# Optimization experiments

Hardware: AMD Instinct MI355X
Metric: run time of the kernel (lower is better)

## Reference

```python
import jax, jax.numpy as jnp
import numpy as np

N = 50000          # num nodes
E = 800000         # num edges
NEG_SLOPE = 0.2    # leaky relu slope for attention logits


def gat_layer(h, W, al, ar, src, dst, res_W=None, res_identity=False, apply_elu=False):
    """One GATConv layer (DGL semantics, dropout=0, fc bias-free).
    h: [N, F_in]; W: [F_in, H*D]; al, ar: [H, D]. Returns [N, H, D]."""
    H, D = al.shape
    feat = (h @ W).reshape(N, H, D)                      # projected features
    el = jnp.sum(feat * al, axis=-1)                     # [N, H]
    er = jnp.sum(feat * ar, axis=-1)                     # [N, H]
    e = jax.nn.leaky_relu(el[src] + er[dst], NEG_SLOPE)  # [E, H] edge logits
    # numerically-stable edge softmax segmented over destination nodes
    m = jax.ops.segment_max(e, dst, num_segments=N)      # [N, H]
    m = jnp.where(jnp.isfinite(m), m, 0.0)               # nodes with no in-edges
    ex = jnp.exp(e - m[dst])
    den = jax.ops.segment_sum(ex, dst, num_segments=N)   # [N, H]
    alpha = ex / (den[dst] + 1e-9)                       # [E, H]
    # message passing: gather src feats, weight by alpha, scatter-add to dst
    out = jax.ops.segment_sum(feat[src] * alpha[..., None], dst, num_segments=N)
    if res_identity:
        out = out + h.reshape(N, H, D)
    elif res_W is not None:
        out = out + (h @ res_W).reshape(N, H, D)
    if apply_elu:
        out = jax.nn.elu(out)
    return out


def setup_inputs() -> dict:
    key = jax.random.key(0)
    ks = jax.random.split(key, 14)
    s = 0.1  # keep attention logits tame
    return {
        "features": jax.random.normal(ks[0], (N, 128), jnp.float32),
        "W0": jax.random.normal(ks[1], (128, 128), jnp.float32) * s,
        "al0": jax.random.normal(ks[2], (4, 32), jnp.float32) * s,
        "ar0": jax.random.normal(ks[3], (4, 32), jnp.float32) * s,
        "W1": jax.random.normal(ks[4], (128, 128), jnp.float32) * s,
        "al1": jax.random.normal(ks[5], (4, 32), jnp.float32) * s,
        "ar1": jax.random.normal(ks[6], (4, 32), jnp.float32) * s,
        "W2": jax.random.normal(ks[7], (128, 40), jnp.float32) * s,
        "al2": jax.random.normal(ks[8], (1, 40), jnp.float32) * s,
        "ar2": jax.random.normal(ks[9], (1, 40), jnp.float32) * s,
        "resW2": jax.random.normal(ks[10], (128, 40), jnp.float32) * s,
        "src": jax.random.randint(ks[11], (E,), 0, N, jnp.int32),
        "dst": jax.random.randint(ks[12], (E,), 0, N, jnp.int32),
    }


def reference(features, W0, al0, ar0, W1, al1, ar1, W2, al2, ar2, resW2, src, dst):
    # hidden layer 0: no residual, elu, flatten heads
    h = gat_layer(features, W0, al0, ar0, src, dst, apply_elu=True).reshape(N, -1)
    # hidden layer 1: residual (identity since in == heads*out), elu, flatten
    h = gat_layer(h, W1, al1, ar1, src, dst, res_identity=True, apply_elu=True).reshape(N, -1)
    # output layer: residual projection, no activation, mean over heads
    logits = gat_layer(h, W2, al2, ar2, src, dst, res_W=resW2).mean(axis=1)
    return logits
```

## Files before the change

### kernel.cpp

```cpp
#include <hip/hip_runtime.h>
#include <hip/hip_fp16.h>

#define NNODES 50000
#define NEDGES 800000
#define NBUCK 196
#define NCHUNK 256
#define CHUNK 3125

typedef _Float16 f16x8 __attribute__((ext_vector_type(8)));
typedef float f32x4 __attribute__((ext_vector_type(4)));


__global__ __launch_bounds__(256) void k_packhist(const int* __restrict__ src,
                                                  const int* __restrict__ dst,
                                                  unsigned* __restrict__ pack,
                                                  int* __restrict__ hist) {
  __shared__ int h[NBUCK];
  int t = threadIdx.x, c = blockIdx.x;
  for (int i = t; i < NBUCK; i += 256) h[i] = 0;
  __syncthreads();
  int beg = c * CHUNK;
  for (int q = t; q < CHUNK; q += 256) {
    int e = beg + q;
    unsigned d = (unsigned)dst[e], sv = (unsigned)src[e];
    pack[e] = (d << 16) | sv;
    atomicAdd(&h[d >> 8], 1);
  }
  __syncthreads();
  for (int i = t; i < NBUCK; i += 256) hist[i * NCHUNK + c] = h[i];
}

__global__ __launch_bounds__(1024) void k_scanall(const int* __restrict__ hist,
                                                  int* __restrict__ off) {
  __shared__ int sb[1024];
  int t = threadIdx.x;
  const int P = (NBUCK * NCHUNK) / 1024;
  int base = t * P;
  int s = 0;
  for (int i = 0; i < P; ++i) s += hist[base + i];
  sb[t] = s;
  __syncthreads();
  for (int o = 1; o < 1024; o <<= 1) {
    int x = (t >= o) ? sb[t - o] : 0;
    __syncthreads();
    sb[t] += x;
    __syncthreads();
  }
  int ex = sb[t] - s;
  for (int i = 0; i < P; ++i) {
    int v = hist[base + i];
    off[base + i] = ex;
    ex += v;
  }
}

__global__ __launch_bounds__(256) void k_partition(const unsigned* __restrict__ pack,
                                                   const int* __restrict__ off,
                                                   unsigned* __restrict__ bucketed) {
  __shared__ int cur[NBUCK];
  int t = threadIdx.x, c = blockIdx.x;
  for (int i = t; i < NBUCK; i += 256) cur[i] = off[i * NCHUNK + c];
  __syncthreads();
  int beg = c * CHUNK;
  for (int q = t; q < CHUNK; q += 256) {
    unsigned v = pack[beg + q];
    int pos = atomicAdd(&cur[v >> 24], 1);
    bucketed[pos] = v;
  }
}

__global__ __launch_bounds__(256) void k_sortbkt(const unsigned* __restrict__ bucketed,
                                                 const int* __restrict__ off,
                                                 int* __restrict__ row_off,
                                                 int* __restrict__ esrc) {
  __shared__ int cnt[256];
  __shared__ int cur[256];
  int t = threadIdx.x, b = blockIdx.x;
  int base = off[b * NCHUNK];
  int endb = (b == NBUCK - 1) ? NEDGES : off[(b + 1) * NCHUNK];
  int ne = endb - base;
  cnt[t] = 0;
  __syncthreads();
  for (int i = t; i < ne; i += 256)
    atomicAdd(&cnt[(bucketed[base + i] >> 16) & 255], 1);
  __syncthreads();
  int orig = cnt[t];
  cur[t] = orig;
  __syncthreads();
  for (int o = 1; o < 256; o <<= 1) {
    int x = (t >= o) ? cur[t - o] : 0;
    __syncthreads();
    cur[t] += x;
    __syncthreads();
  }
  int excl = cur[t] - orig;
  int g = (b << 8) + t;
  if (g <= NNODES) row_off[g] = base + excl;
  cur[t] = excl;
  __syncthreads();
  for (int i = t; i < ne; i += 256) {
    unsigned v = bucketed[base + i];
    int pos = base + atomicAdd(&cur[(v >> 16) & 255], 1);
    esrc[pos] = (int)(v & 0xFFFFu);
  }
}

__global__ __launch_bounds__(128) void k_prep(const float* __restrict__ W0, const float* __restrict__ al0,
                                              const float* __restrict__ ar0,
                                              const float* __restrict__ W1, const float* __restrict__ al1,
                                              const float* __restrict__ ar1,
                                              const float* __restrict__ W2, const float* __restrict__ resW2,
                                              const float* __restrict__ al2, const float* __restrict__ ar2,
                                              _Float16* __restrict__ Wt0, _Float16* __restrict__ Wt1,
                                              _Float16* __restrict__ Wt2) {
  int b = blockIdx.x, k = threadIdx.x;
  if (b < 288) {
    const float* W = (b < 144) ? W0 : W1;
    const float* al = (b < 144) ? al0 : al1;
    const float* ar = (b < 144) ? ar0 : ar1;
    _Float16* Wt = (b < 144) ? Wt0 : Wt1;
    int c = (b < 144) ? b : b - 144;
    float v = 0.f;
    if (c < 128) {
      v = W[k * 128 + c];
    } else if (c < 136) {
      int h = c - 128;
      const float* av = (h < 4) ? al : ar;
      int hh = h & 3;
      float s = 0.f;
      for (int d = 0; d < 32; ++d) s += W[k * 128 + hh * 32 + d] * av[hh * 32 + d];
      v = s;
    }
    Wt[c * 128 + k] = (_Float16)v;
  } else {
    int c = b - 288;
    float v = 0.f;
    if (c < 40) {
      v = W2[k * 40 + c];
    } else if (c < 80) {
      v = resW2[k * 40 + (c - 40)];
    } else if (c == 80) {
      float s = 0.f;
      for (int d = 0; d < 40; ++d) s += W2[k * 40 + d] * al2[d];
      v = s;
    } else if (c == 81) {
      float s = 0.f;
      for (int d = 0; d < 40; ++d) s += W2[k * 40 + d] * ar2[d];
      v = s;
    }
    Wt2[c * 128 + k] = (_Float16)v;
  }
}

template <int NCT, bool L2E, bool AF32>
__global__ __launch_bounds__(512) void k_gemm_mfma(const void* __restrict__ Av,
                                                   const _Float16* __restrict__ Wtg,
                                                   __half* __restrict__ C,
                                                   float* __restrict__ resOut,
                                                   float* __restrict__ el,
                                                   float* __restrict__ er, int nrows) {
  __shared__ _Float16 Ah[128 * 136];
  __shared__ _Float16 Wl[NCT * 16 * 136];
  int t = threadIdx.x;
  int r0 = blockIdx.x * 128;

  for (int q = t; q < NCT * 16 * 16; q += 512) {
    int row = q >> 4, k8 = (q & 15) * 8;
    *(f16x8*)(&Wl[row * 136 + k8]) = *(const f16x8*)(Wtg + row * 128 + k8);
  }
  if (AF32) {
    const float* A = (const float*)Av;
    #pragma unroll
    for (int p = 0; p < 8; ++p) {
      int q = p * 512 + t;
      int r = q >> 5, k4 = (q & 31) * 4;
      float4 v = make_float4(0.f, 0.f, 0.f, 0.f);
      if (r0 + r < nrows) v = *(const float4*)(A + (size_t)(r0 + r) * 128 + k4);
      union { _Float16 h[4]; uint2 u; } pk;
      pk.h[0] = (_Float16)v.x; pk.h[1] = (_Float16)v.y;
      pk.h[2] = (_Float16)v.z; pk.h[3] = (_Float16)v.w;
      *(uint2*)(&Ah[r * 136 + k4]) = pk.u;
    }
  } else {
    const __half* A = (const __half*)Av;
    #pragma unroll
    for (int p = 0; p < 4; ++p) {
      int q = p * 512 + t;
      int r = q >> 4, k8 = (q & 15) * 8;
      union { f16x8 v; uint4 u; } pk;
      pk.u = make_uint4(0, 0, 0, 0);
      if (r0 + r < nrows) pk.v = *(const f16x8*)(A + (size_t)(r0 + r) * 128 + k8);
      *(f16x8*)(&Ah[r * 136 + k8]) = pk.v;
    }
  }
  __syncthreads();

  int wave = t >> 6, l = t & 63;
  const _Float16* abase = &Ah[(wave * 16 + (l & 15)) * 136 + ((l >> 4) * 8)];
  const _Float16* bbase = &Wl[(l & 15) * 136 + ((l >> 4) * 8)];

  f32x4 acc[NCT] = {};
  #pragma unroll
  for (int ks = 0; ks < 4; ++ks) {
    f16x8 af = *(const f16x8*)(abase + ks * 32);
    #pragma unroll
    for (int nt = 0; nt < NCT; ++nt) {
      f16x8 bf = *(const f16x8*)(bbase + nt * 16 * 136 + ks * 32);
      acc[nt] = __builtin_amdgcn_mfma_f32_16x16x32_f16(af, bf, acc[nt], 0, 0, 0);
    }
  }

  int cc = l & 15;
  int rbase = r0 + wave * 16 + (l >> 4) * 4;
  #pragma unroll
  for (int r = 0; r < 4; ++r) {
    int row = rbase + r;
    if (row >= nrows) continue;
    if (!L2E) {
      #pragma unroll
      for (int nt = 0; nt < 8; ++nt)
        C[(size_t)row * 128 + nt * 16 + cc] = __float2half_rn(acc[nt][r]);
      float v = acc[8][r];
      if (cc < 4) el[row * 4 + cc] = v;
      else if (cc < 8) er[row * 4 + (cc - 4)] = v;
    } else {
      #pragma unroll
      for (int nt = 0; nt < 6; ++nt) {
        int col = nt * 16 + cc;
        float v = acc[nt][r];
        if (col < 40) C[(size_t)row * 40 + col] = __float2half_rn(v);
        else if (col < 80) resOut[(size_t)row * 40 + (col - 40)] = v;
        else if (col == 80) el[row] = v;
        else if (col == 81) er[row] = v;
      }
    }
  }
}

__device__ __forceinline__ void fma8h(float4& a0, float4& a1, float w, const uint4& r) {
  const __half* hp = (const __half*)&r;
  a0.x += w * __half2float(hp[0]);
  a0.y += w * __half2float(hp[1]);
  a0.z += w * __half2float(hp[2]);
  a0.w += w * __half2float(hp[3]);
  a1.x += w * __half2float(hp[4]);
  a1.y += w * __half2float(hp[5]);
  a1.z += w * __half2float(hp[6]);
  a1.w += w * __half2float(hp[7]);
}

template <bool RES, bool DOELU>
__global__ __launch_bounds__(256) void k_msg128v5(const __half* __restrict__ feat,
                                                  const float* __restrict__ el,
                                                  const float* __restrict__ er,
                                                  const int* __restrict__ row_off,
                                                  const int* __restrict__ esrc,
                                                  const __half* __restrict__ hres,
                                                  __half* __restrict__ out, int nnodes) {
  int t = threadIdx.x;
  int n = blockIdx.x * 16 + (t >> 4);
  if (n >= nnodes) return;
  int lane = t & 15;
  int h = lane >> 2;
  int s = row_off[n], e = row_off[n + 1];
  float ern = er[n * 4 + h];
  float4 acc0[4] = {}, acc1[4] = {};
  float dpart = 0.f;
  int hb = h << 2;

  for (int c = s; c < e; c += 16) {
    int m = e - c; if (m > 16) m = 16;
    int sjl = (lane < m) ? esrc[c + lane] : 0;
    int b0 = lane & 3;
    int e0 = __shfl(sjl, b0, 16);
    int e1 = __shfl(sjl, b0 + 4, 16);
    int e2 = __shfl(sjl, b0 + 8, 16);
    int e3 = __shfl(sjl, b0 + 12, 16);
    float x0 = el[e0 * 4 + h] + ern;
    float x1 = el[e1 * 4 + h] + ern;
    float x2 = el[e2 * 4 + h] + ern;
    float x3 = el[e3 * 4 + h] + ern;
    x0 = fmaxf(x0, 0.2f * x0);
    x1 = fmaxf(x1, 0.2f * x1);
    x2 = fmaxf(x2, 0.2f * x2);
    x3 = fmaxf(x3, 0.2f * x3);
    float w0 = (b0 < m) ? __expf(x0) : 0.f;
    float w1 = (b0 + 4 < m) ? __expf(x1) : 0.f;
    float w2 = (b0 + 8 < m) ? __expf(x2) : 0.f;
    float w3 = (b0 + 12 < m) ? __expf(x3) : 0.f;
    dpart += (w0 + w1) + (w2 + w3);

#define GAT_J(J, WK)                                                          \
    if (J < m) {                                                              \
      float wgt = __shfl(WK, hb | (J & 3), 16);                               \
      int sj = __shfl(sjl, J, 16);                                            \
      uint4 raw = *(const uint4*)(feat + (size_t)sj * 128 + lane * 8);        \
      fma8h(acc0[J & 3], acc1[J & 3], wgt, raw);                              \
    }
    GAT_J(0, w0) GAT_J(1, w0) GAT_J(2, w0) GAT_J(3, w0)
    GAT_J(4, w1) GAT_J(5, w1) GAT_J(6, w1) GAT_J(7, w1)
    GAT_J(8, w2) GAT_J(9, w2) GAT_J(10, w2) GAT_J(11, w2)
    GAT_J(12, w3) GAT_J(13, w3) GAT_J(14, w3) GAT_J(15, w3)
#undef GAT_J
  }

  float den = dpart;
  den += __shfl_xor(den, 1, 16);
  den += __shfl_xor(den, 2, 16);

  float4 A0, A1;
  A0.x = (acc0[0].x + acc0[1].x) + (acc0[2].x + acc0[3].x);
  A0.y = (acc0[0].y + acc0[1].y) + (acc0[2].y + acc0[3].y);
  A0.z = (acc0[0].z + acc0[1].z) + (acc0[2].z + acc0[3].z);
  A0.w = (acc0[0].w + acc0[1].w) + (acc0[2].w + acc0[3].w);
  A1.x = (acc1[0].x + acc1[1].x) + (acc1[2].x + acc1[3].x);
  A1.y = (acc1[0].y + acc1[1].y) + (acc1[2].y + acc1[3].y);
  A1.z = (acc1[0].z + acc1[1].z) + (acc1[2].z + acc1[3].z);
  A1.w = (acc1[0].w + acc1[1].w) + (acc1[2].w + acc1[3].w);
  float inv = (e > s) ? 1.f / den : 0.f;
  A0.x *= inv; A0.y *= inv; A0.z *= inv; A0.w *= inv;
  A1.x *= inv; A1.y *= inv; A1.z *= inv; A1.w *= inv;
  if (RES) {
    uint4 rr = *(const uint4*)(hres + (size_t)n * 128 + lane * 8);
    const __half* hp = (const __half*)&rr;
    A0.x += __half2float(hp[0]); A0.y += __half2float(hp[1]);
    A0.z += __half2float(hp[2]); A0.w += __half2float(hp[3]);
    A1.x += __half2float(hp[4]); A1.y += __half2float(hp[5]);
    A1.z += __half2float(hp[6]); A1.w += __half2float(hp[7]);
  }
  if (DOELU) {
    A0.x = (A0.x > 0.f) ? A0.x : expm1f(A0.x);
    A0.y = (A0.y > 0.f) ? A0.y : expm1f(A0.y);
    A0.z = (A0.z > 0.f) ? A0.z : expm1f(A0.z);
    A0.w = (A0.w > 0.f) ? A0.w : expm1f(A0.w);
    A1.x = (A1.x > 0.f) ? A1.x : expm1f(A1.x);
    A1.y = (A1.y > 0.f) ? A1.y : expm1f(A1.y);
    A1.z = (A1.z > 0.f) ? A1.z : expm1f(A1.z);
    A1.w = (A1.w > 0.f) ? A1.w : expm1f(A1.w);
  }
  union { __half hh[8]; uint4 u; } pk;
  pk.hh[0] = __float2half_rn(A0.x); pk.hh[1] = __float2half_rn(A0.y);
  pk.hh[2] = __float2half_rn(A0.z); pk.hh[3] = __float2half_rn(A0.w);
  pk.hh[4] = __float2half_rn(A1.x); pk.hh[5] = __float2half_rn(A1.y);
  pk.hh[6] = __float2half_rn(A1.z); pk.hh[7] = __float2half_rn(A1.w);
  *(uint4*)(out + (size_t)n * 128 + lane * 8) = pk.u;
}

__global__ __launch_bounds__(256) void k_msg40v5(const __half* __restrict__ feat,
                                                 const float* __restrict__ el,
                                                 const float* __restrict__ er,
                                                 const int* __restrict__ row_off,
                                                 const int* __restrict__ esrc,
                                                 const float* __restrict__ res,
                                                 float* __restrict__ out, int nnodes) {
  int t = threadIdx.x;
  int n = blockIdx.x * 16 + (t >> 4);
  if (n >= nnodes) return;
  int lane = t & 15;
  int s = row_off[n], e = row_off[n + 1];
  float ern = er[n];
  float4 acc[2] = {};
  float dpart = 0.f;

  for (int c = s; c < e; c += 16) {
    int m = e - c; if (m > 16) m = 16;
    int sjl = (lane < m) ? esrc[c + lane] : 0;
    float x = el[sjl] + ern;
    x = fmaxf(x, 0.2f * x);
    float wl = (lane < m) ? __expf(x) : 0.f;
    dpart += wl;
    #pragma unroll
    for (int j = 0; j < 16; ++j) {
      if (j < m) {
        float wgt = __shfl(wl, j, 16);
        int sj = __shfl(sjl, j, 16);
        if (lane < 10) {
          uint2 raw = *(const uint2*)(feat + (size_t)sj * 40 + lane * 4);
          const __half2* hp = (const __half2*)&raw;
          float2 f0 = __half22float2(hp[0]);
          float2 f1 = __half22float2(hp[1]);
          acc[j & 1].x += wgt * f0.x;
          acc[j & 1].y += wgt * f0.y;
          acc[j & 1].z += wgt * f1.x;
          acc[j & 1].w += wgt * f1.y;
        }
      }
    }
  }
  float den = dpart;
  den += __shfl_xor(den, 1, 16);
  den += __shfl_xor(den, 2, 16);
  den += __shfl_xor(den, 4, 16);
  den += __shfl_xor(den, 8, 16);
  float inv = (e > s) ? 1.f / den : 0.f;
  if (lane < 10) {
    float4 r = *(const float4*)(res + (size_t)n * 40 + lane * 4);
    float4 A;
    A.x = (acc[0].x + acc[1].x) * inv + r.x;
    A.y = (acc[0].y + acc[1].y) * inv + r.y;
    A.z = (acc[0].z + acc[1].z) * inv + r.z;
    A.w = (acc[0].w + acc[1].w) * inv + r.w;
    *(float4*)(out + (size_t)n * 40 + lane * 4) = A;
  }
}

extern "C" void kernel_launch(void* const* d_in, const int* in_sizes, int n_in,
                              void* d_out, int out_size, void* d_ws, size_t ws_size,
                              hipStream_t stream) {
  const float* features = (const float*)d_in[0];
  const float* W0 = (const float*)d_in[1];
  const float* al0 = (const float*)d_in[2];
  const float* ar0 = (const float*)d_in[3];
  const float* W1 = (const float*)d_in[4];
  const float* al1 = (const float*)d_in[5];
  const float* ar1 = (const float*)d_in[6];
  const float* W2 = (const float*)d_in[7];
  const float* al2 = (const float*)d_in[8];
  const float* ar2 = (const float*)d_in[9];
  const float* resW2 = (const float*)d_in[10];
  const int* src = (const int*)d_in[11];
  const int* dst = (const int*)d_in[12];
  float* out = (float*)d_out;

  const int N = NNODES;
  char* w = (char*)d_ws;
  auto alloc = [&](size_t bytes) {
    char* p = w;
    w += (bytes + 255) & ~(size_t)255;
    return p;
  };
  int* row_off = (int*)alloc((size_t)(N + 1) * 4);
  int* esrc = (int*)alloc((size_t)NEDGES * 4);
  unsigned* pack = (unsigned*)alloc((size_t)NEDGES * 4);
  unsigned* bucketed = (unsigned*)alloc((size_t)NEDGES * 4);
  int* hist = (int*)alloc(NBUCK * NCHUNK * 4);
  int* off = (int*)alloc(NBUCK * NCHUNK * 4);
  __half* feath = (__half*)alloc((size_t)N * 128 * 2);
  float* res2 = (float*)alloc((size_t)N * 40 * 4);
  float* el = (float*)alloc((size_t)N * 4 * 4);
  float* er = (float*)alloc((size_t)N * 4 * 4);
  __half* h1 = (__half*)alloc((size_t)N * 128 * 2);
  __half* h2 = (__half*)alloc((size_t)N * 128 * 2);
  _Float16* Wt0 = (_Float16*)alloc(144 * 128 * 2);
  _Float16* Wt1 = (_Float16*)alloc(144 * 128 * 2);
  _Float16* Wt2 = (_Float16*)alloc(96 * 128 * 2);
  __half* feat2h = feath;

  k_prep<<<384, 128, 0, stream>>>(W0, al0, ar0, W1, al1, ar1, W2, resW2, al2, ar2,
                                  Wt0, Wt1, Wt2);

  k_packhist<<<NCHUNK, 256, 0, stream>>>(src, dst, pack, hist);
  k_scanall<<<1, 1024, 0, stream>>>(hist, off);
  k_partition<<<NCHUNK, 256, 0, stream>>>(pack, off, bucketed);
  k_sortbkt<<<NBUCK, 256, 0, stream>>>(bucketed, off, row_off, esrc);

  const int GB128 = (N + 127) / 128;
  const int GM = (N + 15) / 16;

  k_gemm_mfma<9, false, true><<<GB128, 512, 0, stream>>>(features, Wt0, feath, nullptr, el, er, N);
  k_msg128v5<false, true><<<GM, 256, 0, stream>>>(feath, el, er, row_off, esrc, nullptr, h1, N);

  k_gemm_mfma<9, false, false><<<GB128, 512, 0, stream>>>(h1, Wt1, feath, nullptr, el, er, N);
  k_msg128v5<true, true><<<GM, 256, 0, stream>>>(feath, el, er, row_off, esrc, h1, h2, N);

  k_gemm_mfma<6, true, false><<<GB128, 512, 0, stream>>>(h2, Wt2, feat2h, res2, el, er, N);
  k_msg40v5<<<GM, 256, 0, stream>>>(feat2h, el, er, row_off, esrc, res2, out, N);
}
```

Before: 203.7 us.

## Precompute edge attention weights in separate edge-parallel kernels and batch feature loads

Adds per-layer edge kernels that compute exp(leaky_relu(el[src]+er[dst])) once per edge and store the results as fp16 in a head-major buffer. The sorted edge array now keeps the packed src/dst word so dst is available to these kernels. The message kernels read the precomputed weights instead of gathering el and computing exp. They also issue eight feature loads up front before the FMAs to raise memory-level parallelism. The cost is three extra launches, an extra write and read of the weight buffer, and fp16 rounding of the attention weights.

```diff
diff --git a/kernel.cpp b/kernel.cpp
--- a/kernel.cpp
+++ b/kernel.cpp
@@ -72,7 +72,7 @@
 __global__ __launch_bounds__(256) void k_sortbkt(const unsigned* __restrict__ bucketed,
                                                  const int* __restrict__ off,
                                                  int* __restrict__ row_off,
-                                                 int* __restrict__ esrc) {
+                                                 unsigned* __restrict__ epack) {
   __shared__ int cnt[256];
   __shared__ int cur[256];
   int t = threadIdx.x, b = blockIdx.x;
@@ -101,7 +101,7 @@
   for (int i = t; i < ne; i += 256) {
     unsigned v = bucketed[base + i];
     int pos = base + atomicAdd(&cur[(v >> 16) & 255], 1);
-    esrc[pos] = (int)(v & 0xFFFFu);
+    epack[pos] = v;
   }
 }
 
@@ -152,6 +152,37 @@
   }
 }
 
+__global__ __launch_bounds__(256) void k_wedge4(const float* __restrict__ el,
+                                                const float* __restrict__ er,
+                                                const unsigned* __restrict__ epack,
+                                                __half* __restrict__ wbuf) {
+  int e = blockIdx.x * 256 + threadIdx.x;
+  if (e >= NEDGES) return;
+  unsigned v = epack[e];
+  int s = (int)(v & 0xFFFFu), d = (int)(v >> 16);
+  float4 l = *(const float4*)(el + (size_t)s * 4);
+  float4 r = *(const float4*)(er + (size_t)d * 4);
+  float x0 = l.x + r.x, x1 = l.y + r.y, x2 = l.z + r.z, x3 = l.w + r.w;
+  x0 = fmaxf(x0, 0.2f * x0); x1 = fmaxf(x1, 0.2f * x1);
+  x2 = fmaxf(x2, 0.2f * x2); x3 = fmaxf(x3, 0.2f * x3);
+  wbuf[0 * NEDGES + e] = __float2half_rn(__expf(x0));
+  wbuf[1 * NEDGES + e] = __float2half_rn(__expf(x1));
+  wbuf[2 * NEDGES + e] = __float2half_rn(__expf(x2));
+  wbuf[3 * NEDGES + e] = __float2half_rn(__expf(x3));
+}
+
+__global__ __launch_bounds__(256) void k_wedge1(const float* __restrict__ el,
+                                                const float* __restrict__ er,
+                                                const unsigned* __restrict__ epack,
+                                                __half* __restrict__ wbuf) {
+  int e = blockIdx.x * 256 + threadIdx.x;
+  if (e >= NEDGES) return;
+  unsigned v = epack[e];
+  float x = el[v & 0xFFFFu] + er[v >> 16];
+  x = fmaxf(x, 0.2f * x);
+  wbuf[e] = __float2half_rn(__expf(x));
+}
+
 template <int NCT, bool L2E, bool AF32>
 __global__ __launch_bounds__(512) void k_gemm_mfma(const void* __restrict__ Av,
                                                    const _Float16* __restrict__ Wtg,
@@ -250,11 +281,10 @@
 }
 
 template <bool RES, bool DOELU>
-__global__ __launch_bounds__(256) void k_msg128v5(const __half* __restrict__ feat,
-                                                  const float* __restrict__ el,
-                                                  const float* __restrict__ er,
+__global__ __launch_bounds__(256) void k_msg128v6(const __half* __restrict__ feat,
+                                                  const __half* __restrict__ wbuf,
                                                   const int* __restrict__ row_off,
-                                                  const int* __restrict__ esrc,
+                                                  const unsigned* __restrict__ epack,
                                                   const __half* __restrict__ hres,
                                                   __half* __restrict__ out, int nnodes) {
   int t = threadIdx.x;
@@ -262,46 +292,47 @@
   if (n >= nnodes) return;
   int lane = t & 15;
   int h = lane >> 2;
+  int b0 = lane & 3;
+  int hb = h << 2;
   int s = row_off[n], e = row_off[n + 1];
-  float ern = er[n * 4 + h];
+  const __half* whp = wbuf + (size_t)h * NEDGES;
   float4 acc0[4] = {}, acc1[4] = {};
   float dpart = 0.f;
-  int hb = h << 2;
 
   for (int c = s; c < e; c += 16) {
     int m = e - c; if (m > 16) m = 16;
-    int sjl = (lane < m) ? esrc[c + lane] : 0;
-    int b0 = lane & 3;
-    int e0 = __shfl(sjl, b0, 16);
-    int e1 = __shfl(sjl, b0 + 4, 16);
-    int e2 = __shfl(sjl, b0 + 8, 16);
-    int e3 = __shfl(sjl, b0 + 12, 16);
-    float x0 = el[e0 * 4 + h] + ern;
-    float x1 = el[e1 * 4 + h] + ern;
-    float x2 = el[e2 * 4 + h] + ern;
-    float x3 = el[e3 * 4 + h] + ern;
-    x0 = fmaxf(x0, 0.2f * x0);
-    x1 = fmaxf(x1, 0.2f * x1);
-    x2 = fmaxf(x2, 0.2f * x2);
-    x3 = fmaxf(x3, 0.2f * x3);
-    float w0 = (b0 < m) ? __expf(x0) : 0.f;
-    float w1 = (b0 + 4 < m) ? __expf(x1) : 0.f;
-    float w2 = (b0 + 8 < m) ? __expf(x2) : 0.f;
-    float w3 = (b0 + 12 < m) ? __expf(x3) : 0.f;
+    int sjl = (lane < m) ? (int)(epack[c + lane] & 0xFFFFu) : 0;
+    float w0 = (b0 < m) ? __half2float(whp[c + b0]) : 0.f;
+    float w1 = (b0 + 4 < m) ? __half2float(whp[c + b0 + 4]) : 0.f;
+    float w2 = (b0 + 8 < m) ? __half2float(whp[c + b0 + 8]) : 0.f;
+    float w3 = (b0 + 12 < m) ? __half2float(whp[c + b0 + 12]) : 0.f;
     dpart += (w0 + w1) + (w2 + w3);
 
-#define GAT_J(J, WK)                                                          \
+#define GAT_LD(J)                                                             \
+    uint4 r##J = make_uint4(0, 0, 0, 0);                                      \
+    if (J < m) {                                                              \
+      int sj = __shfl(sjl, J, 16);                                            \
+      r##J = *(const uint4*)(feat + (size_t)sj * 128 + lane * 8);             \
+    }
+#define GAT_FM(J, WK)                                                         \
     if (J < m) {                                                              \
       float wgt = __shfl(WK, hb | (J & 3), 16);                               \
-      int sj = __shfl(sjl, J, 16);                                            \
-      uint4 raw = *(const uint4*)(feat + (size_t)sj * 128 + lane * 8);        \
-      fma8h(acc0[J & 3], acc1[J & 3], wgt, raw);                              \
-    }
-    GAT_J(0, w0) GAT_J(1, w0) GAT_J(2, w0) GAT_J(3, w0)
-    GAT_J(4, w1) GAT_J(5, w1) GAT_J(6, w1) GAT_J(7, w1)
-    GAT_J(8, w2) GAT_J(9, w2) GAT_J(10, w2) GAT_J(11, w2)
-    GAT_J(12, w3) GAT_J(13, w3) GAT_J(14, w3) GAT_J(15, w3)
-#undef GAT_J
+      fma8h(acc0[J & 3], acc1[J & 3], wgt, r##J);                             \
+    }
+    {
+      GAT_LD(0) GAT_LD(1) GAT_LD(2) GAT_LD(3)
+      GAT_LD(4) GAT_LD(5) GAT_LD(6) GAT_LD(7)
+      GAT_FM(0, w0) GAT_FM(1, w0) GAT_FM(2, w0) GAT_FM(3, w0)
+      GAT_FM(4, w1) GAT_FM(5, w1) GAT_FM(6, w1) GAT_FM(7, w1)
+    }
+    if (m > 8) {
+      GAT_LD(8) GAT_LD(9) GAT_LD(10) GAT_LD(11)
+      GAT_LD(12) GAT_LD(13) GAT_LD(14) GAT_LD(15)
+      GAT_FM(8, w2) GAT_FM(9, w2) GAT_FM(10, w2) GAT_FM(11, w2)
+      GAT_FM(12, w3) GAT_FM(13, w3) GAT_FM(14, w3) GAT_FM(15, w3)
+    }
+#undef GAT_LD
+#undef GAT_FM
   }
 
   float den = dpart;
@@ -346,11 +377,10 @@
   *(uint4*)(out + (size_t)n * 128 + lane * 8) = pk.u;
 }
 
-__global__ __launch_bounds__(256) void k_msg40v5(const __half* __restrict__ feat,
-                                                 const float* __restrict__ el,
-                                                 const float* __restrict__ er,
+__global__ __launch_bounds__(256) void k_msg40v6(const __half* __restrict__ feat,
+                                                 const __half* __restrict__ wbuf,
                                                  const int* __restrict__ row_off,
-                                                 const int* __restrict__ esrc,
+                                                 const unsigned* __restrict__ epack,
                                                  const float* __restrict__ res,
                                                  float* __restrict__ out, int nnodes) {
   int t = threadIdx.x;
@@ -358,16 +388,13 @@
   if (n >= nnodes) return;
   int lane = t & 15;
   int s = row_off[n], e = row_off[n + 1];
-  float ern = er[n];
   float4 acc[2] = {};
   float dpart = 0.f;
 
   for (int c = s; c < e; c += 16) {
     int m = e - c; if (m > 16) m = 16;
-    int sjl = (lane < m) ? esrc[c + lane] : 0;
-    float x = el[sjl] + ern;
-    x = fmaxf(x, 0.2f * x);
-    float wl = (lane < m) ? __expf(x) : 0.f;
+    int sjl = (lane < m) ? (int)(epack[c + lane] & 0xFFFFu) : 0;
+    float wl = (lane < m) ? __half2float(wbuf[c + lane]) : 0.f;
     dpart += wl;
     #pragma unroll
     for (int j = 0; j < 16; ++j) {
@@ -430,12 +457,13 @@
     return p;
   };
   int* row_off = (int*)alloc((size_t)(N + 1) * 4);
-  int* esrc = (int*)alloc((size_t)NEDGES * 4);
+  unsigned* epack = (unsigned*)alloc((size_t)NEDGES * 4);
   unsigned* pack = (unsigned*)alloc((size_t)NEDGES * 4);
   unsigned* bucketed = (unsigned*)alloc((size_t)NEDGES * 4);
   int* hist = (int*)alloc(NBUCK * NCHUNK * 4);
   int* off = (int*)alloc(NBUCK * NCHUNK * 4);
   __half* feath = (__half*)alloc((size_t)N * 128 * 2);
+  __half* wbuf = (__half*)alloc((size_t)4 * NEDGES * 2);
   float* res2 = (float*)alloc((size_t)N * 40 * 4);
   float* el = (float*)alloc((size_t)N * 4 * 4);
   float* er = (float*)alloc((size_t)N * 4 * 4);
@@ -452,17 +480,21 @@
   k_packhist<<<NCHUNK, 256, 0, stream>>>(src, dst, pack, hist);
   k_scanall<<<1, 1024, 0, stream>>>(hist, off);
   k_partition<<<NCHUNK, 256, 0, stream>>>(pack, off, bucketed);
-  k_sortbkt<<<NBUCK, 256, 0, stream>>>(bucketed, off, row_off, esrc);
+  k_sortbkt<<<NBUCK, 256, 0, stream>>>(bucketed, off, row_off, epack);
 
   const int GB128 = (N + 127) / 128;
   const int GM = (N + 15) / 16;
+  const int GE = (NEDGES + 255) / 256;
 
   k_gemm_mfma<9, false, true><<<GB128, 512, 0, stream>>>(features, Wt0, feath, nullptr, el, er, N);
-  k_msg128v5<false, true><<<GM, 256, 0, stream>>>(feath, el, er, row_off, esrc, nullptr, h1, N);
+  k_wedge4<<<GE, 256, 0, stream>>>(el, er, epack, wbuf);
+  k_msg128v6<false, true><<<GM, 256, 0, stream>>>(feath, wbuf, row_off, epack, nullptr, h1, N);
 
   k_gemm_mfma<9, false, false><<<GB128, 512, 0, stream>>>(h1, Wt1, feath, nullptr, el, er, N);
-  k_msg128v5<true, true><<<GM, 256, 0, stream>>>(feath, el, er, row_off, esrc, h1, h2, N);
+  k_wedge4<<<GE, 256, 0, stream>>>(el, er, epack, wbuf);
+  k_msg128v6<true, true><<<GM, 256, 0, stream>>>(feath, wbuf, row_off, epack, h1, h2, N);
 
   k_gemm_mfma<6, true, false><<<GB128, 512, 0, stream>>>(h2, Wt2, feat2h, res2, el, er, N);
-  k_msg40v5<<<GM, 256, 0, stream>>>(feat2h, el, er, row_off, esrc, res2, out, N);
-}
+  k_wedge1<<<GE, 256, 0, stream>>>(el, er, epack, wbuf);
+  k_msg40v6<<<GM, 256, 0, stream>>>(feat2h, wbuf, row_off, epack, res2, out, N);
+}
```

Result: slower. 260.4 us (+27.9%).

## Split 128-wide GAT aggregation across per-head blocks with 8-lane node groups

Applied to the files above, without the earlier changes.

Replaces the 16-lane-per-node message kernel with a version where each block handles one head slice (32 features) for 32 nodes, using 8 lanes per node and 8-byte gathers. Each lane computes one edge's attention weight for its own head directly, which removes the 4-way shuffle-and-recompute of weights and cuts register use. This trades one wide 256-byte row gather per edge for four 64-byte gathers issued from different blocks, and each edge's source index and logit are now loaded four times.

```diff
diff --git a/kernel.cpp b/kernel.cpp
--- a/kernel.cpp
+++ b/kernel.cpp
@@ -9,7 +9,6 @@
 
 typedef _Float16 f16x8 __attribute__((ext_vector_type(8)));
 typedef float f32x4 __attribute__((ext_vector_type(4)));
-
 
 __global__ __launch_bounds__(256) void k_packhist(const int* __restrict__ src,
                                                   const int* __restrict__ dst,
@@ -237,20 +236,8 @@
   }
 }
 
-__device__ __forceinline__ void fma8h(float4& a0, float4& a1, float w, const uint4& r) {
-  const __half* hp = (const __half*)&r;
-  a0.x += w * __half2float(hp[0]);
-  a0.y += w * __half2float(hp[1]);
-  a0.z += w * __half2float(hp[2]);
-  a0.w += w * __half2float(hp[3]);
-  a1.x += w * __half2float(hp[4]);
-  a1.y += w * __half2float(hp[5]);
-  a1.z += w * __half2float(hp[6]);
-  a1.w += w * __half2float(hp[7]);
-}
-
 template <bool RES, bool DOELU>
-__global__ __launch_bounds__(256) void k_msg128v5(const __half* __restrict__ feat,
+__global__ __launch_bounds__(256) void k_msg128v8(const __half* __restrict__ feat,
                                                   const float* __restrict__ el,
                                                   const float* __restrict__ er,
                                                   const int* __restrict__ row_off,
@@ -258,92 +245,68 @@
                                                   const __half* __restrict__ hres,
                                                   __half* __restrict__ out, int nnodes) {
   int t = threadIdx.x;
-  int n = blockIdx.x * 16 + (t >> 4);
+  int slice = blockIdx.x & 3;
+  int nb = blockIdx.x >> 2;
+  int n = nb * 32 + (t >> 3);
   if (n >= nnodes) return;
-  int lane = t & 15;
-  int h = lane >> 2;
+  int lane = t & 7;
   int s = row_off[n], e = row_off[n + 1];
-  float ern = er[n * 4 + h];
-  float4 acc0[4] = {}, acc1[4] = {};
+  float ern = er[n * 4 + slice];
+  const __half* fbase = feat + slice * 32 + lane * 4;
+  float4 acc[2] = {};
   float dpart = 0.f;
-  int hb = h << 2;
-
-  for (int c = s; c < e; c += 16) {
-    int m = e - c; if (m > 16) m = 16;
+
+  for (int c = s; c < e; c += 8) {
+    int m = e - c; if (m > 8) m = 8;
     int sjl = (lane < m) ? esrc[c + lane] : 0;
-    int b0 = lane & 3;
-    int e0 = __shfl(sjl, b0, 16);
-    int e1 = __shfl(sjl, b0 + 4, 16);
-    int e2 = __shfl(sjl, b0 + 8, 16);
-    int e3 = __shfl(sjl, b0 + 12, 16);
-    float x0 = el[e0 * 4 + h] + ern;
-    float x1 = el[e1 * 4 + h] + ern;
-    float x2 = el[e2 * 4 + h] + ern;
-    float x3 = el[e3 * 4 + h] + ern;
-    x0 = fmaxf(x0, 0.2f * x0);
-    x1 = fmaxf(x1, 0.2f * x1);
-    x2 = fmaxf(x2, 0.2f * x2);
-    x3 = fmaxf(x3, 0.2f * x3);
-    float w0 = (b0 < m) ? __expf(x0) : 0.f;
-    float w1 = (b0 + 4 < m) ? __expf(x1) : 0.f;
-    float w2 = (b0 + 8 < m) ? __expf(x2) : 0.f;
-    float w3 = (b0 + 12 < m) ? __expf(x3) : 0.f;
-    dpart += (w0 + w1) + (w2 + w3);
-
-#define GAT_J(J, WK)                                                          \
-    if (J < m) {                                                              \
-      float wgt = __shfl(WK, hb | (J & 3), 16);                               \
-      int sj = __shfl(sjl, J, 16);                                            \
-      uint4 raw = *(const uint4*)(feat + (size_t)sj * 128 + lane * 8);        \
-      fma8h(acc0[J & 3], acc1[J & 3], wgt, raw);                              \
-    }
-    GAT_J(0, w0) GAT_J(1, w0) GAT_J(2, w0) GAT_J(3, w0)
-    GAT_J(4, w1) GAT_J(5, w1) GAT_J(6, w1) GAT_J(7, w1)
-    GAT_J(8, w2) GAT_J(9, w2) GAT_J(10, w2) GAT_J(11, w2)
-    GAT_J(12, w3) GAT_J(13, w3) GAT_J(14, w3) GAT_J(15, w3)
-#undef GAT_J
+    float x = el[sjl * 4 + slice] + ern;
+    x = fmaxf(x, 0.2f * x);
+    float wl = (lane < m) ? __expf(x) : 0.f;
+    dpart += wl;
+    #pragma unroll
+    for (int j = 0; j < 8; ++j) {
+      if (j < m) {
+        float wgt = __shfl(wl, j, 8);
+        int sj = __shfl(sjl, j, 8);
+        uint2 raw = *(const uint2*)(fbase + (size_t)sj * 128);
+        const __half2* hp = (const __half2*)&raw;
+        float2 f0 = __half22float2(hp[0]);
+        float2 f1 = __half22float2(hp[1]);
+        acc[j & 1].x += wgt * f0.x;
+        acc[j & 1].y += wgt * f0.y;
+        acc[j & 1].z += wgt * f1.x;
+        acc[j & 1].w += wgt * f1.y;
+      }
+    }
   }
 
   float den = dpart;
-  den += __shfl_xor(den, 1, 16);
-  den += __shfl_xor(den, 2, 16);
-
-  float4 A0, A1;
-  A0.x = (acc0[0].x + acc0[1].x) + (acc0[2].x + acc0[3].x);
-  A0.y = (acc0[0].y + acc0[1].y) + (acc0[2].y + acc0[3].y);
-  A0.z = (acc0[0].z + acc0[1].z) + (acc0[2].z + acc0[3].z);
-  A0.w = (acc0[0].w + acc0[1].w) + (acc0[2].w + acc0[3].w);
-  A1.x = (acc1[0].x + acc1[1].x) + (acc1[2].x + acc1[3].x);
-  A1.y = (acc1[0].y + acc1[1].y) + (acc1[2].y + acc1[3].y);
-  A1.z = (acc1[0].z + acc1[1].z) + (acc1[2].z + acc1[3].z);
-  A1.w = (acc1[0].w + acc1[1].w) + (acc1[2].w + acc1[3].w);
+  den += __shfl_xor(den, 1, 8);
+  den += __shfl_xor(den, 2, 8);
+  den += __shfl_xor(den, 4, 8);
   float inv = (e > s) ? 1.f / den : 0.f;
-  A0.x *= inv; A0.y *= inv; A0.z *= inv; A0.w *= inv;
-  A1.x *= inv; A1.y *= inv; A1.z *= inv; A1.w *= inv;
+  float4 A;
+  A.x = (acc[0].x + acc[1].x) * inv;
+  A.y = (acc[0].y + acc[1].y) * inv;
+  A.z = (acc[0].z + acc[1].z) * inv;
+  A.w = (acc[0].w + acc[1].w) * inv;
+  size_t obase = (size_t)n * 128 + slice * 32 + lane * 4;
   if (RES) {
-    uint4 rr = *(const uint4*)(hres + (size_t)n * 128 + lane * 8);
+    uint2 rr = *(const uint2*)(hres + obase);
     const __half* hp = (const __half*)&rr;
-    A0.x += __half2float(hp[0]); A0.y += __half2float(hp[1]);
-    A0.z += __half2float(hp[2]); A0.w += __half2float(hp[3]);
-    A1.x += __half2float(hp[4]); A1.y += __half2float(hp[5]);
-    A1.z += __half2float(hp[6]); A1.w += __half2float(hp[7]);
+    A.x += __half2float(hp[0]); A.y += __half2float(hp[1]);
+    A.z += __half2float(hp[2]); A.w += __half2float(hp[3]);
   }
   if (DOELU) {
-    A0.x = (A0.x > 0.f) ? A0.x : expm1f(A0.x);
-    A0.y = (A0.y > 0.f) ? A0.y : expm1f(A0.y);
-    A0.z = (A0.z > 0.f) ? A0.z : expm1f(A0.z);
-    A0.w = (A0.w > 0.f) ? A0.w : expm1f(A0.w);
-    A1.x = (A1.x > 0.f) ? A1.x : expm1f(A1.x);
-    A1.y = (A1.y > 0.f) ? A1.y : expm1f(A1.y);
-    A1.z = (A1.z > 0.f) ? A1.z : expm1f(A1.z);
-    A1.w = (A1.w > 0.f) ? A1.w : expm1f(A1.w);
-  }
-  union { __half hh[8]; uint4 u; } pk;
-  pk.hh[0] = __float2half_rn(A0.x); pk.hh[1] = __float2half_rn(A0.y);
-  pk.hh[2] = __float2half_rn(A0.z); pk.hh[3] = __float2half_rn(A0.w);
-  pk.hh[4] = __float2half_rn(A1.x); pk.hh[5] = __float2half_rn(A1.y);
-  pk.hh[6] = __float2half_rn(A1.z); pk.hh[7] = __float2half_rn(A1.w);
-  *(uint4*)(out + (size_t)n * 128 + lane * 8) = pk.u;
+    A.x = (A.x > 0.f) ? A.x : expm1f(A.x);
+    A.y = (A.y > 0.f) ? A.y : expm1f(A.y);
+    A.z = (A.z > 0.f) ? A.z : expm1f(A.z);
+    A.w = (A.w > 0.f) ? A.w : expm1f(A.w);
+  }
+  union { __half hh[4]; uint2 u; } pk;
+  pk.hh[0] = __float2half_rn(A.x); pk.hh[1] = __float2half_rn(A.y);
+  pk.hh[2] = __float2half_rn(A.z); pk.hh[3] = __float2half_rn(A.w);
+  *(uint2*)(out + obase) = pk.u;
 }
 
 __global__ __launch_bounds__(256) void k_msg40v5(const __half* __restrict__ feat,
@@ -455,13 +418,14 @@
   k_sortbkt<<<NBUCK, 256, 0, stream>>>(bucketed, off, row_off, esrc);
 
   const int GB128 = (N + 127) / 128;
+  const int GM8 = ((N + 31) / 32) * 4;
   const int GM = (N + 15) / 16;
 
   k_gemm_mfma<9, false, true><<<GB128, 512, 0, stream>>>(features, Wt0, feath, nullptr, el, er, N);
-  k_msg128v5<false, true><<<GM, 256, 0, stream>>>(feath, el, er, row_off, esrc, nullptr, h1, N);
+  k_msg128v8<false, true><<<GM8, 256, 0, stream>>>(feath, el, er, row_off, esrc, nullptr, h1, N);
 
   k_gemm_mfma<9, false, false><<<GB128, 512, 0, stream>>>(h1, Wt1, feath, nullptr, el, er, N);
-  k_msg128v5<true, true><<<GM, 256, 0, stream>>>(feath, el, er, row_off, esrc, h1, h2, N);
+  k_msg128v8<true, true><<<GM8, 256, 0, stream>>>(feath, el, er, row_off, esrc, h1, h2, N);
 
   k_gemm_mfma<6, true, false><<<GB128, 512, 0, stream>>>(h2, Wt2, feat2h, res2, el, er, N);
   k_msg40v5<<<GM, 256, 0, stream>>>(feat2h, el, er, row_off, esrc, res2, out, N);
```

After: 243.8 us. +19.7%, slower.
